# Optimization experiments

Hardware: AMD Instinct MI355X
Metric: run time of the kernel (lower is better)

## Reference

```python
import jax, jax.numpy as jnp
import numpy as np

B, K, DIM = 65536, 512, 128
EPS = 1e-8
LN_2PI = 1.83787706641


def setup_inputs() -> dict:
    key = jax.random.key(0)
    k1, k2, k3 = jax.random.split(key, 3)
    x = jax.random.normal(k1, (B, DIM), dtype=jnp.float32)
    centers = jax.random.uniform(k2, (K, DIM), dtype=jnp.float32)
    # torch init: 0.2 * rand + 0.9
    D_param = 0.2 * jax.random.uniform(k3, (K, DIM), dtype=jnp.float32) + 0.9
    return {"x": x, "centers": centers, "D_param": D_param}


def reference(x, centers, D_param):
    Bc, dim = x.shape
    Kc = centers.shape[0]
    Dabs = jnp.abs(D_param) + EPS          # [K, D]
    Dinv = 1.0 / Dabs                       # diagonal Sigma^{-1}
    log_det = jnp.sum(jnp.log(Dabs), axis=1)  # [K]
    dsf = -0.5 * log_det
    det_scale_safe = jnp.exp(dsf - jnp.max(dsf))  # [K]

    # dist_sq[b,k] = sum_d (x[b,d]-c[k,d])^2 * Dinv[k,d], via GEMM expansion
    # (avoids the [B,K,D] diff tensor the torch loop materializes)
    dist_sq = ((x * x) @ Dinv.T
               - 2.0 * (x @ (centers * Dinv).T)
               + jnp.sum(centers * centers * Dinv, axis=1)[None, :])  # [B, K]

    expo_gmm = -0.5 * dist_sq
    expo_cmm = jnp.power(dist_sq + 1.0, -((1.0 + dim) / 2.0))

    def log_resp(expo):
        safe = expo - jnp.max(expo, axis=-1, keepdims=True)
        numer = det_scale_safe[None, :] * jnp.exp(safe)
        denom = jnp.sum(numer, axis=1, keepdims=True)
        return jnp.log(jnp.clip(numer / denom, 1e-8))

    resp_gmm = log_resp(expo_gmm)
    resp_cmm = log_resp(expo_cmm)

    assign = jnp.argmax(resp_gmm, axis=1)                    # [B]
    onehot = jax.nn.one_hot(assign, Kc, dtype=expo_gmm.dtype)  # [B, K]
    ce = -0.5 * dim * LN_2PI + log_det[None, :] + expo_gmm
    # torch multiplies onehot twice; onehot^2 == onehot
    ce = (-1.0 / Bc) * jnp.sum(onehot * ce)

    # return_gmm and return_cmm both True
    a = jax.nn.softmax(resp_gmm, axis=-1)
    b = jax.nn.softmax(resp_cmm, axis=-1)
    resp = jnp.log((a + b) / 2.0)
    return resp, ce
```

## Files before the change

### kernel.cpp

```cpp
#include <hip/hip_runtime.h>
#include <math.h>

#define NROWS 65536
#define KCL   512
#define NDIM  128
#define CE_IDX ((size_t)NROWS * (size_t)KCL)
#define LN_2PI 1.83787706641f

using f32x4  = __attribute__((ext_vector_type(4))) float;
using short8 = __attribute__((ext_vector_type(8))) short;

__device__ __forceinline__ unsigned short f2bf(float f) {
    unsigned u = __float_as_uint(f);
    return (unsigned short)((u + 0x7fffu + ((u >> 16) & 1u)) >> 16);
}

__device__ __forceinline__ unsigned cvt_pk_bf16(float lo, float hi) {
    unsigned r;
    asm("v_cvt_pk_bf16_f32 %0, %1, %2" : "=v"(r) : "v"(lo), "v"(hi));
    return r;
}

__global__ void k_prep(const float* __restrict__ centers,
                       const float* __restrict__ Dp,
                       unsigned short* __restrict__ W,
                       float* __restrict__ log_det,
                       float* __restrict__ cdotc) {
    int n = blockIdx.x;
    int d = threadIdx.x;
    int t = n >> 4, m = n & 15;
    float Dabs = fabsf(Dp[n * NDIM + d]) + 1e-8f;
    float dinv = 1.0f / Dabs;
    float c = centers[n * NDIM + d];
    int j1 = d, j2 = 128 + d;
    W[t * 4096 + (j1 >> 3) * 128 + m * 8 + (j1 & 7)] = f2bf(-2.0f * c * dinv);
    W[t * 4096 + (j2 >> 3) * 128 + m * 8 + (j2 & 7)] = f2bf(dinv);
    float lg = logf(Dabs);
    float cc = c * c * dinv;
    #pragma unroll
    for (int s = 32; s >= 1; s >>= 1) {
        lg += __shfl_xor(lg, s);
        cc += __shfl_xor(cc, s);
    }
    __shared__ float sred[4];
    if ((d & 63) == 0) { sred[(d >> 6) * 2 + 0] = lg; sred[(d >> 6) * 2 + 1] = cc; }
    __syncthreads();
    if (d == 0) { log_det[n] = sred[0] + sred[2]; cdotc[n] = sred[1] + sred[3]; }
}

__global__ void k_scale(const float* __restrict__ log_det,
                        float* __restrict__ dss,
                        float* __restrict__ inv_sum,
                        float* __restrict__ ce_slot) {
    int k = threadIdx.x;
    float dsf = -0.5f * log_det[k];
    float m = dsf;
    #pragma unroll
    for (int s = 32; s >= 1; s >>= 1) m = fmaxf(m, __shfl_xor(m, s));
    __shared__ float sm[KCL / 64], ss[KCL / 64];
    if ((k & 63) == 0) sm[k >> 6] = m;
    __syncthreads();
    float mm = sm[0];
    #pragma unroll
    for (int i = 1; i < KCL / 64; i++) mm = fmaxf(mm, sm[i]);
    float v = __expf(dsf - mm);
    dss[k] = v;
    float s = v;
    #pragma unroll
    for (int sh = 32; sh >= 1; sh >>= 1) s += __shfl_xor(s, sh);
    if ((k & 63) == 0) ss[k >> 6] = s;
    __syncthreads();
    if (k == 0) {
        float tot = 0.0f;
        #pragma unroll
        for (int i = 0; i < KCL / 64; i++) tot += ss[i];
        *inv_sum = 1.0f / tot;
        *ce_slot = 0.0f;
    }
}

__global__ __launch_bounds__(256) __attribute__((amdgpu_waves_per_eu(3, 8)))
void k_main(const float* __restrict__ x,
            const unsigned short* __restrict__ W,
            const float* __restrict__ log_det,
            const float* __restrict__ cdotc,
            const float* __restrict__ dss,
            const float* __restrict__ inv_sum,
            float* __restrict__ out) {
    __shared__ float s_cd[KCL], s_ld[KCL], s_ds[KCL];
    __shared__ float ex_mn[4][16], ex_key[4][16], ex_ds[4][16], ex_sg[4][16];

    const int tid = threadIdx.x;
    s_cd[tid] = cdotc[tid];   s_cd[tid + 256] = cdotc[tid + 256];
    s_ld[tid] = log_det[tid]; s_ld[tid + 256] = log_det[tid + 256];
    s_ds[tid] = dss[tid];     s_ds[tid + 256] = dss[tid + 256];

    const int lane = tid & 63;
    const int w = __builtin_amdgcn_readfirstlane(tid >> 6);
    const int m = lane & 15;
    const int q = lane >> 4;
    const int r0 = blockIdx.x * 16;

    const float* xp = x + (size_t)(r0 + m) * NDIM + q * 8;
    short8 afx[4], afxx[4];
    #pragma unroll
    for (int kk = 0; kk < 4; kk++) {
        float4 a0 = *(const float4*)(xp + kk * 32);
        float4 a1 = *(const float4*)(xp + kk * 32 + 4);
        union { unsigned u[4]; short8 s; } A, AX;
        A.u[0]  = cvt_pk_bf16(a0.x, a0.y);
        A.u[1]  = cvt_pk_bf16(a0.z, a0.w);
        A.u[2]  = cvt_pk_bf16(a1.x, a1.y);
        A.u[3]  = cvt_pk_bf16(a1.z, a1.w);
        AX.u[0] = cvt_pk_bf16(a0.x * a0.x, a0.y * a0.y);
        AX.u[1] = cvt_pk_bf16(a0.z * a0.z, a0.w * a0.w);
        AX.u[2] = cvt_pk_bf16(a1.x * a1.x, a1.y * a1.y);
        AX.u[3] = cvt_pk_bf16(a1.z * a1.z, a1.w * a1.w);
        afx[kk] = A.s; afxx[kk] = AX.s;
    }

    f32x4 acc[8];
    #pragma unroll
    for (int v = 0; v < 8; v++) acc[v] = (f32x4){0.f, 0.f, 0.f, 0.f};

    const unsigned short* gWq = W + ((size_t)w * 8) * 4096 + lane * 8;
    #pragma unroll
    for (int v = 0; v < 8; v++) {
        const unsigned short* tb = gWq + v * 4096;
        #pragma unroll
        for (int kk = 0; kk < 4; kk++) {
            short8 b0 = *(const short8*)(tb + kk * 512);
            short8 b1 = *(const short8*)(tb + 2048 + kk * 512);
            acc[v] = __builtin_amdgcn_mfma_f32_16x16x32_bf16(afx[kk],  b0, acc[v], 0, 0, 0);
            acc[v] = __builtin_amdgcn_mfma_f32_16x16x32_bf16(afxx[kk], b1, acc[v], 0, 0, 0);
        }
    }

    __syncthreads();

    const int colbase = w * 128 + m;
    float mn[4], bkey[4], bds[4];
    #pragma unroll
    for (int r = 0; r < 4; r++) { mn[r] = INFINITY; bkey[r] = INFINITY; bds[r] = 0.f; }
    #pragma unroll
    for (int v = 0; v < 8; v++) {
        const int col = colbase + v * 16;
        float cd = s_cd[col], ldc = s_ld[col];
        #pragma unroll
        for (int r = 0; r < 4; r++) {
            float ds = acc[v][r] + cd;
            acc[v][r] = ds;
            mn[r] = fminf(mn[r], ds);
            float key = ds + ldc;
            bool t = key < bkey[r];
            bkey[r] = t ? key : bkey[r];
            bds[r]  = t ? ds  : bds[r];
        }
    }
    #pragma unroll
    for (int s = 1; s < 16; s <<= 1) {
        #pragma unroll
        for (int r = 0; r < 4; r++) {
            mn[r] = fminf(mn[r], __shfl_xor(mn[r], s));
            float ok = __shfl_xor(bkey[r], s);
            float od = __shfl_xor(bds[r],  s);
            bool t = ok < bkey[r];
            bkey[r] = t ? ok : bkey[r];
            bds[r]  = t ? od : bds[r];
        }
    }
    if (m == 0) {
        #pragma unroll
        for (int r = 0; r < 4; r++) {
            ex_mn[w][q * 4 + r]  = mn[r];
            ex_key[w][q * 4 + r] = bkey[r];
            ex_ds[w][q * 4 + r]  = bds[r];
        }
    }
    __syncthreads();

    float hmn[4], pay[4], Sg[4];
    #pragma unroll
    for (int r = 0; r < 4; r++) {
        const int row = q * 4 + r;
        float g0 = fminf(ex_mn[0][row], ex_mn[1][row]);
        float g1 = fminf(ex_mn[2][row], ex_mn[3][row]);
        hmn[r] = 0.5f * fminf(g0, g1);
        float bk = ex_key[0][row], bd = ex_ds[0][row];
        #pragma unroll
        for (int w2 = 1; w2 < 4; w2++) {
            float ok = ex_key[w2][row], od = ex_ds[w2][row];
            bool t = ok < bk;
            bk = t ? ok : bk;
            bd = t ? od : bd;
        }
        pay[r] = fmaf(-1.5f, bd, bk);
        Sg[r] = 0.f;
    }

    float dsv[8];
    #pragma unroll
    for (int v = 0; v < 8; v++) {
        dsv[v] = s_ds[colbase + v * 16];
        #pragma unroll
        for (int r = 0; r < 4; r++) {
            float ng = dsv[v] * __expf(fmaf(-0.5f, acc[v][r], hmn[r]));
            Sg[r] += ng;
            acc[v][r] = ng;
        }
    }
    #pragma unroll
    for (int s = 1; s < 16; s <<= 1)
        #pragma unroll
        for (int r = 0; r < 4; r++) Sg[r] += __shfl_xor(Sg[r], s);

    if (m == 0) {
        #pragma unroll
        for (int r = 0; r < 4; r++) ex_sg[w][q * 4 + r] = Sg[r];
    }
    __syncthreads();

    const float isum05 = 0.5f * (*inv_sum);
    float iSg05[4];
    #pragma unroll
    for (int r = 0; r < 4; r++) {
        const int row = q * 4 + r;
        float st = (ex_sg[0][row] + ex_sg[1][row]) + (ex_sg[2][row] + ex_sg[3][row]);
        iSg05[r] = 0.5f / st;
    }

    #pragma unroll
    for (int v = 0; v < 8; v++) {
        float bt = dsv[v] * isum05;
        #pragma unroll
        for (int r = 0; r < 4; r++) {
            float z = fmaxf(acc[v][r] * iSg05[r], 5e-9f) + bt;
            out[(size_t)(r0 + q * 4 + r) * KCL + colbase + v * 16] = __logf(z);
        }
    }

    if (w == 0) {
        float ce = (pay[0] + pay[1]) + (pay[2] + pay[3]);
        if (m != 0) ce = 0.0f;
        ce += __shfl_xor(ce, 16);
        ce += __shfl_xor(ce, 32);
        if (lane == 0) {
            float vv = (-1.0f / (float)NROWS) *
                       (ce + 16.0f * (-0.5f * (float)NDIM * LN_2PI));
            atomicAdd(out + CE_IDX, vv);
        }
    }
}

extern "C" void kernel_launch(void* const* d_in, const int* in_sizes, int n_in,
                              void* d_out, int out_size, void* d_ws, size_t ws_size,
                              hipStream_t stream) {
    const float* x       = (const float*)d_in[0];
    const float* centers = (const float*)d_in[1];
    const float* Dp      = (const float*)d_in[2];
    float* out = (float*)d_out;

    unsigned short* W = (unsigned short*)d_ws;
    float* log_det = (float*)((char*)d_ws + (size_t)KCL * 256 * sizeof(unsigned short));
    float* cdotc   = log_det + KCL;
    float* dss     = cdotc + KCL;
    float* inv_sum = dss + KCL;

    k_prep<<<KCL, NDIM, 0, stream>>>(centers, Dp, W, log_det, cdotc);
    k_scale<<<1, KCL, 0, stream>>>(log_det, dss, inv_sum, out + CE_IDX);
    k_main<<<NROWS / 16, 256, 0, stream>>>(x, W, log_det, cdotc, dss, inv_sum, out);
}
```

Baseline: 240.4 us.

## Stage W through LDS with triple-buffered async loads; fold scale kernel into main

Each block now handles 64 rows with 512 threads and streams the bf16 weight matrix through a triple-buffered LDS ring using global_load_lds, so each W tile is fetched once per block instead of once per wave from global memory. The separate k_scale kernel is removed. Its det-scale and normalisation values are recomputed in every main block, and the CE slot is zeroed with a memset. The intent is to cut redundant global and L2 traffic for W and one kernel launch. The cost is more LDS per block (about 48KB), a barrier on every tile, and 16 accumulators per wave, which raises register pressure. The det-scale max subtraction is dropped, which assumes exp(-0.5*log_det) stays in range.

Result: faster. 194.7 us (-19.0%).

```diff
diff --git a/kernel.cpp b/kernel.cpp
--- a/kernel.cpp
+++ b/kernel.cpp
@@ -19,6 +19,13 @@
     unsigned r;
     asm("v_cvt_pk_bf16_f32 %0, %1, %2" : "=v"(r) : "v"(lo), "v"(hi));
     return r;
+}
+
+__device__ __forceinline__ void gld_lds16(const void* g, void* l) {
+    __builtin_amdgcn_global_load_lds(
+        (const __attribute__((address_space(1))) unsigned int*)g,
+        (__attribute__((address_space(3))) unsigned int*)l,
+        16, 0, 0);
 }
 
 __global__ void k_prep(const float* __restrict__ centers,
@@ -48,60 +55,41 @@
     if (d == 0) { log_det[n] = sred[0] + sred[2]; cdotc[n] = sred[1] + sred[3]; }
 }
 
-__global__ void k_scale(const float* __restrict__ log_det,
-                        float* __restrict__ dss,
-                        float* __restrict__ inv_sum,
-                        float* __restrict__ ce_slot) {
-    int k = threadIdx.x;
-    float dsf = -0.5f * log_det[k];
-    float m = dsf;
-    #pragma unroll
-    for (int s = 32; s >= 1; s >>= 1) m = fmaxf(m, __shfl_xor(m, s));
-    __shared__ float sm[KCL / 64], ss[KCL / 64];
-    if ((k & 63) == 0) sm[k >> 6] = m;
-    __syncthreads();
-    float mm = sm[0];
-    #pragma unroll
-    for (int i = 1; i < KCL / 64; i++) mm = fmaxf(mm, sm[i]);
-    float v = __expf(dsf - mm);
-    dss[k] = v;
-    float s = v;
-    #pragma unroll
-    for (int sh = 32; sh >= 1; sh >>= 1) s += __shfl_xor(s, sh);
-    if ((k & 63) == 0) ss[k >> 6] = s;
-    __syncthreads();
-    if (k == 0) {
-        float tot = 0.0f;
-        #pragma unroll
-        for (int i = 0; i < KCL / 64; i++) tot += ss[i];
-        *inv_sum = 1.0f / tot;
-        *ce_slot = 0.0f;
-    }
-}
-
-__global__ __launch_bounds__(256) __attribute__((amdgpu_waves_per_eu(3, 8)))
+__global__ __launch_bounds__(512) __attribute__((amdgpu_waves_per_eu(4, 8)))
 void k_main(const float* __restrict__ x,
             const unsigned short* __restrict__ W,
             const float* __restrict__ log_det,
             const float* __restrict__ cdotc,
-            const float* __restrict__ dss,
-            const float* __restrict__ inv_sum,
             float* __restrict__ out) {
+    __shared__ __align__(16) short ldsW[3][8192];
     __shared__ float s_cd[KCL], s_ld[KCL], s_ds[KCL];
-    __shared__ float ex_mn[4][16], ex_key[4][16], ex_ds[4][16], ex_sg[4][16];
+    __shared__ float ex_mn[2][64], ex_key[2][64], ex_ds[2][64], ex_sg[2][64];
+    __shared__ float sred[8], ce_part[4];
+    __shared__ float s_invsum;
 
     const int tid = threadIdx.x;
-    s_cd[tid] = cdotc[tid];   s_cd[tid + 256] = cdotc[tid + 256];
-    s_ld[tid] = log_det[tid]; s_ld[tid + 256] = log_det[tid + 256];
-    s_ds[tid] = dss[tid];     s_ds[tid + 256] = dss[tid + 256];
+    {
+        float ldv = log_det[tid];
+        float cdv = cdotc[tid];
+        s_ld[tid] = ldv;
+        s_cd[tid] = cdv;
+        float e = __expf(-0.5f * ldv);
+        s_ds[tid] = e;
+        float s = e;
+        #pragma unroll
+        for (int sh = 32; sh >= 1; sh >>= 1) s += __shfl_xor(s, sh);
+        if ((tid & 63) == 0) sred[tid >> 6] = s;
+    }
 
     const int lane = tid & 63;
     const int w = __builtin_amdgcn_readfirstlane(tid >> 6);
+    const int g = w >> 1;
+    const int h = w & 1;
     const int m = lane & 15;
     const int q = lane >> 4;
-    const int r0 = blockIdx.x * 16;
-
-    const float* xp = x + (size_t)(r0 + m) * NDIM + q * 8;
+    const int r0 = blockIdx.x * 64;
+
+    const float* xp = x + (size_t)(r0 + g * 16 + m) * NDIM + q * 8;
     short8 afx[4], afxx[4];
     #pragma unroll
     for (int kk = 0; kk < 4; kk++) {
@@ -119,37 +107,60 @@
         afx[kk] = A.s; afxx[kk] = AX.s;
     }
 
-    f32x4 acc[8];
-    #pragma unroll
-    for (int v = 0; v < 8; v++) acc[v] = (f32x4){0.f, 0.f, 0.f, 0.f};
-
-    const unsigned short* gWq = W + ((size_t)w * 8) * 4096 + lane * 8;
-    #pragma unroll
-    for (int v = 0; v < 8; v++) {
-        const unsigned short* tb = gWq + v * 4096;
+    f32x4 acc[16];
+    #pragma unroll
+    for (int t = 0; t < 16; t++) acc[t] = (f32x4){0.f, 0.f, 0.f, 0.f};
+
+    const char* gWb = (const char*)W + ((w & 4) ? 16 * 8192 : 0)
+                      + (w & 3) * 2048 + (size_t)lane * 16;
+    char* lWb = (char*)&ldsW[0][0] + w * 2048;
+
+    gld_lds16(gWb, lWb);
+    gld_lds16(gWb + 1024, lWb + 1024);
+    __syncthreads();
+
+    if (tid == 0) {
+        float tot = 0.0f;
+        #pragma unroll
+        for (int i = 0; i < 8; i++) tot += sred[i];
+        s_invsum = 1.0f / tot;
+    }
+
+    #pragma unroll
+    for (int u = 0; u < 16; ++u) {
+        if (u < 15) {
+            const char* s = gWb + (size_t)(u + 1) * 8192;
+            char* l = (char*)&ldsW[0][0] + ((u + 1) % 3) * 16384 + w * 2048;
+            gld_lds16(s, l);
+            gld_lds16(s + 1024, l + 1024);
+            asm volatile("s_waitcnt vmcnt(2)" ::: "memory");
+        } else {
+            asm volatile("s_waitcnt vmcnt(0)" ::: "memory");
+        }
+        __builtin_amdgcn_s_barrier();
+        asm volatile("" ::: "memory");
+        const short* lb = &ldsW[u % 3][h * 4096];
         #pragma unroll
         for (int kk = 0; kk < 4; kk++) {
-            short8 b0 = *(const short8*)(tb + kk * 512);
-            short8 b1 = *(const short8*)(tb + 2048 + kk * 512);
-            acc[v] = __builtin_amdgcn_mfma_f32_16x16x32_bf16(afx[kk],  b0, acc[v], 0, 0, 0);
-            acc[v] = __builtin_amdgcn_mfma_f32_16x16x32_bf16(afxx[kk], b1, acc[v], 0, 0, 0);
-        }
-    }
-
-    __syncthreads();
-
-    const int colbase = w * 128 + m;
+            short8 b0 = *(const short8*)(lb + kk * 512 + lane * 8);
+            short8 b1 = *(const short8*)(lb + 2048 + kk * 512 + lane * 8);
+            acc[u] = __builtin_amdgcn_mfma_f32_16x16x32_bf16(afx[kk],  b0, acc[u], 0, 0, 0);
+            acc[u] = __builtin_amdgcn_mfma_f32_16x16x32_bf16(afxx[kk], b1, acc[u], 0, 0, 0);
+        }
+    }
+
+    const int colbase = h * 256 + m;
     float mn[4], bkey[4], bds[4];
     #pragma unroll
     for (int r = 0; r < 4; r++) { mn[r] = INFINITY; bkey[r] = INFINITY; bds[r] = 0.f; }
     #pragma unroll
-    for (int v = 0; v < 8; v++) {
-        const int col = colbase + v * 16;
+    for (int u = 0; u < 16; u++) {
+        const int col = colbase + u * 16;
         float cd = s_cd[col], ldc = s_ld[col];
         #pragma unroll
         for (int r = 0; r < 4; r++) {
-            float ds = acc[v][r] + cd;
-            acc[v][r] = ds;
+            float ds = acc[u][r] + cd;
+            acc[u][r] = ds;
             mn[r] = fminf(mn[r], ds);
             float key = ds + ldc;
             bool t = key < bkey[r];
@@ -169,12 +180,13 @@
             bds[r]  = t ? od : bds[r];
         }
     }
+    const int rowb = g * 16 + q * 4;
     if (m == 0) {
         #pragma unroll
         for (int r = 0; r < 4; r++) {
-            ex_mn[w][q * 4 + r]  = mn[r];
-            ex_key[w][q * 4 + r] = bkey[r];
-            ex_ds[w][q * 4 + r]  = bds[r];
+            ex_mn[h][rowb + r]  = mn[r];
+            ex_key[h][rowb + r] = bkey[r];
+            ex_ds[h][rowb + r]  = bds[r];
         }
     }
     __syncthreads();
@@ -182,31 +194,25 @@
     float hmn[4], pay[4], Sg[4];
     #pragma unroll
     for (int r = 0; r < 4; r++) {
-        const int row = q * 4 + r;
-        float g0 = fminf(ex_mn[0][row], ex_mn[1][row]);
-        float g1 = fminf(ex_mn[2][row], ex_mn[3][row]);
-        hmn[r] = 0.5f * fminf(g0, g1);
-        float bk = ex_key[0][row], bd = ex_ds[0][row];
-        #pragma unroll
-        for (int w2 = 1; w2 < 4; w2++) {
-            float ok = ex_key[w2][row], od = ex_ds[w2][row];
-            bool t = ok < bk;
-            bk = t ? ok : bk;
-            bd = t ? od : bd;
-        }
+        mn[r] = fminf(mn[r], ex_mn[h ^ 1][rowb + r]);
+        float ok = ex_key[h ^ 1][rowb + r];
+        float od = ex_ds[h ^ 1][rowb + r];
+        bool t = h ? (ok <= bkey[r]) : (ok < bkey[r]);
+        float bk = t ? ok : bkey[r];
+        float bd = t ? od : bds[r];
         pay[r] = fmaf(-1.5f, bd, bk);
+        hmn[r] = 0.5f * mn[r];
         Sg[r] = 0.f;
     }
 
-    float dsv[8];
-    #pragma unroll
-    for (int v = 0; v < 8; v++) {
-        dsv[v] = s_ds[colbase + v * 16];
-        #pragma unroll
-        for (int r = 0; r < 4; r++) {
-            float ng = dsv[v] * __expf(fmaf(-0.5f, acc[v][r], hmn[r]));
+    #pragma unroll
+    for (int u = 0; u < 16; u++) {
+        float dsc = s_ds[colbase + u * 16];
+        #pragma unroll
+        for (int r = 0; r < 4; r++) {
+            float ng = dsc * __expf(fmaf(-0.5f, acc[u][r], hmn[r]));
             Sg[r] += ng;
-            acc[v][r] = ng;
+            acc[u][r] = ng;
         }
     }
     #pragma unroll
@@ -216,38 +222,37 @@
 
     if (m == 0) {
         #pragma unroll
-        for (int r = 0; r < 4; r++) ex_sg[w][q * 4 + r] = Sg[r];
-    }
-    __syncthreads();
-
-    const float isum05 = 0.5f * (*inv_sum);
-    float iSg05[4];
-    #pragma unroll
-    for (int r = 0; r < 4; r++) {
-        const int row = q * 4 + r;
-        float st = (ex_sg[0][row] + ex_sg[1][row]) + (ex_sg[2][row] + ex_sg[3][row]);
-        iSg05[r] = 0.5f / st;
-    }
-
-    #pragma unroll
-    for (int v = 0; v < 8; v++) {
-        float bt = dsv[v] * isum05;
-        #pragma unroll
-        for (int r = 0; r < 4; r++) {
-            float z = fmaxf(acc[v][r] * iSg05[r], 5e-9f) + bt;
-            out[(size_t)(r0 + q * 4 + r) * KCL + colbase + v * 16] = __logf(z);
-        }
-    }
-
-    if (w == 0) {
+        for (int r = 0; r < 4; r++) ex_sg[h][rowb + r] = Sg[r];
+    }
+    if (h == 0) {
         float ce = (pay[0] + pay[1]) + (pay[2] + pay[3]);
         if (m != 0) ce = 0.0f;
         ce += __shfl_xor(ce, 16);
         ce += __shfl_xor(ce, 32);
-        if (lane == 0) {
-            float vv = (-1.0f / (float)NROWS) *
-                       (ce + 16.0f * (-0.5f * (float)NDIM * LN_2PI));
-            atomicAdd(out + CE_IDX, vv);
+        if (lane == 0) ce_part[g] = ce;
+    }
+    __syncthreads();
+
+    if (tid == 0) {
+        float ce = (ce_part[0] + ce_part[1]) + (ce_part[2] + ce_part[3]);
+        float v = (-1.0f / (float)NROWS) *
+                  (ce + 64.0f * (-0.5f * (float)NDIM * LN_2PI));
+        atomicAdd(out + CE_IDX, v);
+    }
+
+    float iSg05[4];
+    #pragma unroll
+    for (int r = 0; r < 4; r++)
+        iSg05[r] = 0.5f / (Sg[r] + ex_sg[h ^ 1][rowb + r]);
+
+    const float isum05 = 0.5f * s_invsum;
+    #pragma unroll
+    for (int u = 0; u < 16; u++) {
+        float bt = s_ds[colbase + u * 16] * isum05;
+        #pragma unroll
+        for (int r = 0; r < 4; r++) {
+            float z = fmaxf(acc[u][r] * iSg05[r], 5e-9f) + bt;
+            out[(size_t)(r0 + g * 16 + q * 4 + r) * KCL + colbase + u * 16] = __logf(z);
         }
     }
 }
@@ -263,10 +268,8 @@
     unsigned short* W = (unsigned short*)d_ws;
     float* log_det = (float*)((char*)d_ws + (size_t)KCL * 256 * sizeof(unsigned short));
     float* cdotc   = log_det + KCL;
-    float* dss     = cdotc + KCL;
-    float* inv_sum = dss + KCL;
 
     k_prep<<<KCL, NDIM, 0, stream>>>(centers, Dp, W, log_det, cdotc);
-    k_scale<<<1, KCL, 0, stream>>>(log_det, dss, inv_sum, out + CE_IDX);
-    k_main<<<NROWS / 16, 256, 0, stream>>>(x, W, log_det, cdotc, dss, inv_sum, out);
-}
+    hipMemsetAsync(out + CE_IDX, 0, sizeof(float), stream);
+    k_main<<<NROWS / 64, 512, 0, stream>>>(x, W, log_det, cdotc, out);
+}
```
